# Kernel optimization log

Measured on AMD Instinct MI355X. Metric: run time of the kernel, lower is better.

Reference implementation:

```python
import jax, jax.numpy as jnp
import numpy as np

B, F, V, D, K = 16384, 39, 30000, 16, 20
EPS = 1e-5


def bn_eval(x, g, b):
    # inference-mode BatchNorm1d with running_mean=0, running_var=1
    return g * x / jnp.sqrt(1.0 + EPS) + b


def setup_inputs() -> dict:
    key = jax.random.key(0)
    ks = jax.random.split(key, 12)
    x = jax.random.randint(ks[0], (B, F), 0, V)
    emb_table = jax.random.normal(ks[1], (F * V, D), dtype=jnp.float32) * 0.05
    w_c = jax.random.normal(ks[2], (F, F * D), dtype=jnp.float32) * 0.05
    w0 = jax.random.normal(ks[3], (1024, F * D), dtype=jnp.float32) * 0.04
    w1 = jax.random.normal(ks[4], (512, 1024), dtype=jnp.float32) * 0.03
    w_out = jax.random.normal(ks[5], (1, 512), dtype=jnp.float32) * 0.04
    return {
        'x': x, 'emb_table': emb_table,
        'w_c': w_c, 'b_c': jnp.zeros((F,)), 'g_c': jnp.ones((F,)), 'be_c': jnp.zeros((F,)),
        'w0': w0, 'b0': jnp.zeros((1024,)), 'g0': jnp.ones((1024,)), 'be0': jnp.zeros((1024,)),
        'w1': w1, 'b1': jnp.zeros((512,)), 'g1': jnp.ones((512,)), 'be1': jnp.zeros((512,)),
        'w_out': w_out, 'b_out': jnp.zeros((1,)),
    }


def reference(x, emb_table, w_c, b_c, g_c, be_c, w0, b0, g0, be0,
              w1, b1, g1, be1, w_out, b_out):
    offsets = jnp.arange(F, dtype=x.dtype) * V          # per-field offsets
    idx = x + offsets[None, :]                          # [B, F]
    emb = emb_table[idx]                                # [B, F, D] gather

    # controller_mlp: flatten (batch, D, F) layout like torch transpose(1,2)
    flat = jnp.transpose(emb, (0, 2, 1)).reshape(B, F * D)
    h = jax.nn.relu(bn_eval(flat @ w_c.T + b_c, g_c, be_c))
    scores = jax.nn.softmax(h, axis=1)                  # [B, F]

    # kmax_pooling: top-k field indices, sorted ascending, gather weights
    _, kidx = jax.lax.top_k(scores, K)
    kidx = jnp.sort(kidx, axis=1)                       # [B, K]
    w = jnp.take_along_axis(scores, kidx, axis=1)       # [B, K]

    # forward_select: gather selected field embeddings, weight them
    sel = jnp.take_along_axis(emb, kidx[:, :, None], axis=1)  # [B, K, D]
    weighted = sel * w[:, :, None]

    # scatter back into full field slots (unselected fields are zero)
    full = jnp.zeros((B, F, D), weighted.dtype)
    bidx = jnp.arange(B)[:, None]
    full = full.at[bidx, kidx].set(weighted)            # [B, F, D]

    z = jnp.transpose(full, (0, 2, 1)).reshape(B, F * D)
    z = jax.nn.relu(bn_eval(z @ w0.T + b0, g0, be0))
    z = jax.nn.relu(bn_eval(z @ w1.T + b1, g1, be1))
    out = jax.nn.sigmoid(z @ w_out.T + b_out)           # [B, 1]
    return out.squeeze(-1)
```

## Files before the change

kernel.cpp:

```cpp
#include <hip/hip_runtime.h>
#include <math.h>

#define B_SZ 16384
#define F_N 39
#define V_N 30000
#define D_N 16
#define K_SEL 20
#define FD 624
#define KP0 640
#define NCP 48
#define N0 1024
#define N1 512
#define CBR 16
#define ALD 648

typedef unsigned short u16;
typedef __attribute__((ext_vector_type(8))) short bf16x8;
typedef __attribute__((ext_vector_type(8))) unsigned short u16x8;
typedef __attribute__((ext_vector_type(4))) float f32x4;
typedef __attribute__((ext_vector_type(4))) unsigned short u16x4;

__device__ __forceinline__ u16 f2bf(float v) {
    union { float f; unsigned u; } x; x.f = v;
    unsigned r = x.u + 0x7fff + ((x.u >> 16) & 1);
    return (u16)(r >> 16);
}
__device__ __forceinline__ float bf2f(u16 v) {
    union { unsigned u; float f; } x; x.u = ((unsigned)v) << 16;
    return x.f;
}
__device__ __forceinline__ unsigned cvtpk2(float a, float b) {
    unsigned d;
    asm("v_cvt_pk_bf16_f32 %0, %1, %2" : "=v"(d) : "v"(a), "v"(b));
    return d;
}

#define GLD16(gp, lp) __builtin_amdgcn_global_load_lds( \
    (const __attribute__((address_space(1))) unsigned int*)(gp), \
    (__attribute__((address_space(3))) unsigned int*)(lp), 16, 0, 0)

__global__ __launch_bounds__(256) void prep_all_kernel(
    const float* __restrict__ w0, const float* __restrict__ w1,
    const float* __restrict__ w_c, const float* __restrict__ b_c,
    const float* __restrict__ g_c, const float* __restrict__ be_c,
    u16* __restrict__ w0b, u16* __restrict__ w1b, u16* __restrict__ wcb,
    float* __restrict__ bcp, float* __restrict__ gcp, float* __restrict__ becp,
    float* __restrict__ outp)
{
    __shared__ float Lb[8][624];
    const int bid = blockIdx.x;
    const int t   = threadIdx.x;

    if (bid < 134) {
        const bool is_w0 = (bid < 128);
        const int r0 = is_w0 ? bid * 8 : (bid - 128) * 8;
        const int nrows_src = is_w0 ? N0 : F_N;
        const float* __restrict__ src = is_w0 ? w0 : w_c;
        u16* __restrict__ dst = is_w0 ? w0b : wcb;

        for (int j = t; j < 8 * 156; j += 256) {
            const int row = j / 156;
            const int c4  = j - row * 156;
            const int n   = r0 + row;
            if (n < nrows_src)
                *(float4*)&Lb[row][c4 * 4] =
                    *(const float4*)&src[(size_t)n * FD + c4 * 4];
        }
        __syncthreads();

        for (int j = t; j < 8 * 320; j += 256) {
            const int row = j / 320;
            const int pr  = j - row * 320;
            const int n   = r0 + row;
            const int k0  = pr * 2;
            float v0 = 0.f, v1 = 0.f;
            if (n < nrows_src) {
                const int d0 = k0 & 15,       f0 = k0 >> 4;
                const int d1 = (k0 + 1) & 15, f1 = (k0 + 1) >> 4;
                if (f0 < F_N) v0 = Lb[row][d0 * F_N + f0];
                if (f1 < F_N) v1 = Lb[row][d1 * F_N + f1];
            }
            *(unsigned*)&dst[(size_t)n * KP0 + k0] = cvtpk2(v0, v1);
        }
        return;
    }
    if (bid < 390) {
        const size_t e0 = (size_t)(bid - 134) * 2048 + t * 8;
        float4 v0 = *(const float4*)(w1 + e0);
        float4 v1 = *(const float4*)(w1 + e0 + 4);
        uint4 o = { cvtpk2(v0.x, v0.y), cvtpk2(v0.z, v0.w),
                    cvtpk2(v1.x, v1.y), cvtpk2(v1.z, v1.w) };
        *(uint4*)(w1b + e0) = o;
        return;
    }
    if (bid < 398) {
        const size_t e0 = (size_t)(bid - 390) * 2048 + t * 8;
        float4 z = {0.f, 0.f, 0.f, 0.f};
        *(float4*)(outp + e0)     = z;
        *(float4*)(outp + e0 + 4) = z;
        return;
    }
    if (t < 3 * NCP) {
        const int which = t / NCP, n = t - which * NCP;
        float v = 0.f;
        if (n < F_N) v = (which == 0) ? b_c[n] : (which == 1) ? g_c[n] : be_c[n];
        ((which == 0) ? bcp : (which == 1) ? gcp : becp)[n] = v;
    }
}

__global__ __launch_bounds__(256) void fused_controller_kernel(
    const int* __restrict__ x, const float* __restrict__ emb_table,
    const u16* __restrict__ wcb, const float* __restrict__ bcp,
    const float* __restrict__ gcp, const float* __restrict__ becp,
    u16* __restrict__ zb)
{
    __shared__ __align__(16) u16 Al[CBR * ALD];
    __shared__ float vv[CBR][49];
    __shared__ f32x4 part[4][64][3];
    __shared__ float selw[CBR][F_N];

    const int t    = threadIdx.x;
    const int wave = t >> 6;
    const int lane = t & 63;
    const int b0   = blockIdx.x * CBR;

    {
        const int p0 = t, p1 = t + 256, p2 = t + 512;
        const int xi0 = x[b0 * F_N + p0];
        const int xi1 = x[b0 * F_N + p1];
        const int xi2 = (p2 < CBR * F_N) ? x[b0 * F_N + p2] : 0;
        const int pp[3] = { p0, p1, p2 };
        const int xx[3] = { xi0, xi1, xi2 };
        #pragma unroll
        for (int s = 0; s < 3; ++s) {
            const int p = pp[s];
            if (p < CBR * F_N) {
                const int row = p / F_N;
                const int f   = p - row * F_N;
                const float4* src =
                    (const float4*)(emb_table + (size_t)(xx[s] + f * V_N) * D_N);
                float4 v0 = src[0], v1 = src[1], v2 = src[2], v3 = src[3];
                uint4 o0 = { cvtpk2(v0.x, v0.y), cvtpk2(v0.z, v0.w),
                             cvtpk2(v1.x, v1.y), cvtpk2(v1.z, v1.w) };
                uint4 o1 = { cvtpk2(v2.x, v2.y), cvtpk2(v2.z, v2.w),
                             cvtpk2(v3.x, v3.y), cvtpk2(v3.z, v3.w) };
                *(uint4*)&Al[row * ALD + f * D_N]     = o0;
                *(uint4*)&Al[row * ALD + f * D_N + 8] = o1;
            }
        }
    }
    __syncthreads();

    const int m = lane & 15;
    const int q = lane >> 4;
    f32x4 acc0 = {}, acc1 = {}, acc2 = {};
    {
        const u16* ap  = &Al[m * ALD + wave * 160 + q * 8];
        const u16* bp0 = wcb + (size_t)(0  + m) * KP0 + wave * 160 + q * 8;
        const u16* bp1 = wcb + (size_t)(16 + m) * KP0 + wave * 160 + q * 8;
        const u16* bp2 = wcb + (size_t)(32 + m) * KP0 + wave * 160 + q * 8;
        #pragma unroll
        for (int k = 0; k < 5; ++k) {
            bf16x8 af = *(const bf16x8*)ap;
            bf16x8 b0 = *(const bf16x8*)bp0;
            bf16x8 b1 = *(const bf16x8*)bp1;
            bf16x8 b2 = *(const bf16x8*)bp2;
            acc0 = __builtin_amdgcn_mfma_f32_16x16x32_bf16(af, b0, acc0, 0, 0, 0);
            acc1 = __builtin_amdgcn_mfma_f32_16x16x32_bf16(af, b1, acc1, 0, 0, 0);
            acc2 = __builtin_amdgcn_mfma_f32_16x16x32_bf16(af, b2, acc2, 0, 0, 0);
            ap += 32; bp0 += 32; bp1 += 32; bp2 += 32;
        }
    }
    part[wave][lane][0] = acc0;
    part[wave][lane][1] = acc1;
    part[wave][lane][2] = acc2;
    __syncthreads();

    {
        f32x4 r0 = part[0][lane][0] + part[1][lane][0] + part[2][lane][0] + part[3][lane][0];
        f32x4 r1 = part[0][lane][1] + part[1][lane][1] + part[2][lane][1] + part[3][lane][1];
        f32x4 r2 = part[0][lane][2] + part[1][lane][2] + part[2][lane][2] + part[3][lane][2];

        const float rs = rsqrtf(1.0f + 1e-5f);
        if (q == wave) {
            #pragma unroll
            for (int j = 0; j < 3; ++j) {
                const f32x4 a = (j == 0) ? r0 : (j == 1) ? r1 : r2;
                const int n = j * 16 + m;
                const float gn = gcp[n] * rs;
                const float bn = becp[n];
                const float bi = bcp[n];
                #pragma unroll
                for (int r = 0; r < 4; ++r)
                    vv[wave * 4 + r][n] = fmaxf(fmaf(gn, a[r] + bi, bn), 0.f);
            }
        }
    }
    __syncthreads();

    {
        const int row = wave * 4 + (lane >> 4);
        const int fl  = lane & 15;
        float e[3] = {0.f, 0.f, 0.f};
        float mloc = -1e30f;
        #pragma unroll
        for (int it = 0; it < 3; ++it) {
            const int f = fl + 16 * it;
            if (f < F_N) { e[it] = vv[row][f]; mloc = fmaxf(mloc, e[it]); }
        }
        mloc = fmaxf(mloc, __shfl_xor(mloc, 1, 64));
        mloc = fmaxf(mloc, __shfl_xor(mloc, 2, 64));
        mloc = fmaxf(mloc, __shfl_xor(mloc, 4, 64));
        mloc = fmaxf(mloc, __shfl_xor(mloc, 8, 64));
        float sloc = 0.f;
        #pragma unroll
        for (int it = 0; it < 3; ++it) {
            const int f = fl + 16 * it;
            if (f < F_N) { e[it] = expf(e[it] - mloc); sloc += e[it]; }
        }
        sloc += __shfl_xor(sloc, 1, 64);
        sloc += __shfl_xor(sloc, 2, 64);
        sloc += __shfl_xor(sloc, 4, 64);
        sloc += __shfl_xor(sloc, 8, 64);
        const float inv = 1.f / sloc;
        #pragma unroll
        for (int it = 0; it < 3; ++it) {
            const int f = fl + 16 * it;
            if (f < F_N) vv[row][f] = e[it];
        }

        int rank[3] = {};
        for (int gg = 0; gg < F_N; ++gg) {
            const float o = vv[row][gg];
            #pragma unroll
            for (int it = 0; it < 3; ++it) {
                const int f = fl + 16 * it;
                if (f < F_N)
                    rank[it] += (o > e[it] || (o == e[it] && gg < f)) ? 1 : 0;
            }
        }
        #pragma unroll
        for (int it = 0; it < 3; ++it) {
            const int f = fl + 16 * it;
            if (f < F_N)
                selw[row][f] = (rank[it] < K_SEL) ? e[it] * inv : 0.f;
        }
    }
    __syncthreads();

    for (int gp = t; gp < CBR * 40; gp += 256) {
        const int row  = gp / 40;
        const int slot = gp - row * 40;
        u16* dst = zb + (size_t)(b0 + row) * KP0 + slot * D_N;
        uint4 o0 = {0u,0u,0u,0u}, o1 = {0u,0u,0u,0u};
        if (slot < F_N) {
            const float w = selw[row][slot];
            u16x8 a0 = *(u16x8*)&Al[row * ALD + slot * D_N];
            u16x8 a1 = *(u16x8*)&Al[row * ALD + slot * D_N + 8];
            o0 = (uint4){ cvtpk2(bf2f(a0[0]) * w, bf2f(a0[1]) * w),
                          cvtpk2(bf2f(a0[2]) * w, bf2f(a0[3]) * w),
                          cvtpk2(bf2f(a0[4]) * w, bf2f(a0[5]) * w),
                          cvtpk2(bf2f(a0[6]) * w, bf2f(a0[7]) * w) };
            o1 = (uint4){ cvtpk2(bf2f(a1[0]) * w, bf2f(a1[1]) * w),
                          cvtpk2(bf2f(a1[2]) * w, bf2f(a1[3]) * w),
                          cvtpk2(bf2f(a1[4]) * w, bf2f(a1[5]) * w),
                          cvtpk2(bf2f(a1[6]) * w, bf2f(a1[7]) * w) };
        }
        *(uint4*)dst       = o0;
        *(uint4*)(dst + 8) = o1;
    }
}

template<int MODE>
__global__ __launch_bounds__(512) void gemm_mfma_bn_relu(
    const u16* __restrict__ A, const u16* __restrict__ W,
    const float* __restrict__ bias, const float* __restrict__ g,
    const float* __restrict__ be, u16* __restrict__ Cout,
    int M, int N, int Kp,
    const float* __restrict__ w_out, float* __restrict__ outp)
{
    __shared__ __align__(16) u16 SM[3 * 12288];

    const int t    = threadIdx.x;
    const int wave = t >> 6;
    const int lane = t & 63;
    const int wm   = wave >> 1, wn = wave & 1;
    const int m0   = blockIdx.x * 256;
    const int n0   = blockIdx.y * 128;

    const int rA0 = t >> 2;
    const int cA0 = (t & 3) ^ ((rA0 >> 1) & 3);
    const int rA1 = 128 + rA0;
    const int cA1 = (t & 3) ^ ((rA1 >> 1) & 3);
    const u16* gA0 = A + (size_t)(m0 + rA0) * Kp + cA0 * 8;
    const u16* gA1 = A + (size_t)(m0 + rA1) * Kp + cA1 * 8;
    const u16* gB  = W + (size_t)(n0 + rA0) * Kp + cA0 * 8;
    const int dA0 = t * 8, dA1 = 4096 + t * 8, dB = 8192 + t * 8;

    const int q    = lane >> 4;
    const int lr16 = lane & 15;

    int aoff[4], boff[4];
    #pragma unroll
    for (int i = 0; i < 4; ++i) {
        int ra = wm * 64 + i * 16 + lr16;
        aoff[i] = ra * 32 + ((q ^ ((ra >> 1) & 3)) * 8);
        int rb = wn * 64 + i * 16 + lr16;
        boff[i] = rb * 32 + ((q ^ ((rb >> 1) & 3)) * 8);
    }

    const int NIT = Kp >> 5;

    GLD16(gA0, SM + dA0);
    GLD16(gA1, SM + dA1);
    GLD16(gB,  SM + dB);
    gA0 += 32; gA1 += 32; gB += 32;
    GLD16(gA0, SM + 12288 + dA0);
    GLD16(gA1, SM + 12288 + dA1);
    GLD16(gB,  SM + 12288 + dB);
    gA0 += 32; gA1 += 32; gB += 32;

    f32x4 acc[4][4] = {};
    int cur = 0, stg = 2;

    for (int it = 0; it < NIT - 1; ++it) {
        asm volatile("s_waitcnt vmcnt(3)" ::: "memory");
        __builtin_amdgcn_s_barrier();
        __builtin_amdgcn_sched_barrier(0);

        const u16* ac = SM + cur * 12288;
        const u16* bc = ac + 8192;

        bf16x8 af0 = *(const bf16x8*)(ac + aoff[0]);
        bf16x8 af1 = *(const bf16x8*)(ac + aoff[1]);
        bf16x8 b0v = *(const bf16x8*)(bc + boff[0]);
        bf16x8 b1v = *(const bf16x8*)(bc + boff[1]);
        bf16x8 b2v = *(const bf16x8*)(bc + boff[2]);
        bf16x8 b3v = *(const bf16x8*)(bc + boff[3]);

        if (it + 2 < NIT) {
            u16* s = SM + stg * 12288;
            GLD16(gA0, s + dA0);
            GLD16(gA1, s + dA1);
            GLD16(gB,  s + dB);
            gA0 += 32; gA1 += 32; gB += 32;
        }

        asm volatile("s_waitcnt lgkmcnt(0)" ::: "memory");
        __builtin_amdgcn_sched_barrier(0);
        __builtin_amdgcn_s_setprio(1);
        acc[0][0] = __builtin_amdgcn_mfma_f32_16x16x32_bf16(af0, b0v, acc[0][0], 0, 0, 0);
        acc[0][1] = __builtin_amdgcn_mfma_f32_16x16x32_bf16(af0, b1v, acc[0][1], 0, 0, 0);
        acc[0][2] = __builtin_amdgcn_mfma_f32_16x16x32_bf16(af0, b2v, acc[0][2], 0, 0, 0);
        acc[0][3] = __builtin_amdgcn_mfma_f32_16x16x32_bf16(af0, b3v, acc[0][3], 0, 0, 0);
        acc[1][0] = __builtin_amdgcn_mfma_f32_16x16x32_bf16(af1, b0v, acc[1][0], 0, 0, 0);
        acc[1][1] = __builtin_amdgcn_mfma_f32_16x16x32_bf16(af1, b1v, acc[1][1], 0, 0, 0);
        acc[1][2] = __builtin_amdgcn_mfma_f32_16x16x32_bf16(af1, b2v, acc[1][2], 0, 0, 0);
        acc[1][3] = __builtin_amdgcn_mfma_f32_16x16x32_bf16(af1, b3v, acc[1][3], 0, 0, 0);
        __builtin_amdgcn_s_setprio(0);
        __builtin_amdgcn_s_barrier();

        bf16x8 af2 = *(const bf16x8*)(ac + aoff[2]);
        bf16x8 af3 = *(const bf16x8*)(ac + aoff[3]);
        asm volatile("s_waitcnt lgkmcnt(0)" ::: "memory");
        __builtin_amdgcn_sched_barrier(0);
        __builtin_amdgcn_s_setprio(1);
        acc[2][0] = __builtin_amdgcn_mfma_f32_16x16x32_bf16(af2, b0v, acc[2][0], 0, 0, 0);
        acc[2][1] = __builtin_amdgcn_mfma_f32_16x16x32_bf16(af2, b1v, acc[2][1], 0, 0, 0);
        acc[2][2] = __builtin_amdgcn_mfma_f32_16x16x32_bf16(af2, b2v, acc[2][2], 0, 0, 0);
        acc[2][3] = __builtin_amdgcn_mfma_f32_16x16x32_bf16(af2, b3v, acc[2][3], 0, 0, 0);
        acc[3][0] = __builtin_amdgcn_mfma_f32_16x16x32_bf16(af3, b0v, acc[3][0], 0, 0, 0);
        acc[3][1] = __builtin_amdgcn_mfma_f32_16x16x32_bf16(af3, b1v, acc[3][1], 0, 0, 0);
        acc[3][2] = __builtin_amdgcn_mfma_f32_16x16x32_bf16(af3, b2v, acc[3][2], 0, 0, 0);
        acc[3][3] = __builtin_amdgcn_mfma_f32_16x16x32_bf16(af3, b3v, acc[3][3], 0, 0, 0);
        __builtin_amdgcn_s_setprio(0);

        cur = (cur == 2) ? 0 : cur + 1;
        stg = (stg == 2) ? 0 : stg + 1;
    }

    asm volatile("s_waitcnt vmcnt(0)" ::: "memory");
    __builtin_amdgcn_s_barrier();
    __builtin_amdgcn_sched_barrier(0);
    {
        const u16* ac = SM + cur * 12288;
        const u16* bc = ac + 8192;
        bf16x8 af[4], bfr[4];
        #pragma unroll
        for (int i = 0; i < 4; ++i) af[i]  = *(const bf16x8*)(ac + aoff[i]);
        #pragma unroll
        for (int j = 0; j < 4; ++j) bfr[j] = *(const bf16x8*)(bc + boff[j]);
        __builtin_amdgcn_s_setprio(1);
        #pragma unroll
        for (int i = 0; i < 4; ++i)
            #pragma unroll
            for (int j = 0; j < 4; ++j)
                acc[i][j] = __builtin_amdgcn_mfma_f32_16x16x32_bf16(
                    af[i], bfr[j], acc[i][j], 0, 0, 0);
        __builtin_amdgcn_s_setprio(0);
    }

    const float rs = rsqrtf(1.0f + 1e-5f);
    if (MODE == 0) {
        __syncthreads();
        u16* Cs = SM;
        #pragma unroll
        for (int j = 0; j < 4; ++j) {
            const int nl = wn * 64 + j * 16 + lr16;
            const int n  = n0 + nl;
            const float bn_g = g[n] * rs;
            const float bn_b = be[n];
            const float bi   = bias[n];
            #pragma unroll
            for (int i = 0; i < 4; ++i) {
                const int mlb = wm * 64 + i * 16 + q * 4;
                float v0 = fmaxf(fmaf(bn_g, acc[i][j][0] + bi, bn_b), 0.f);
                float v1 = fmaxf(fmaf(bn_g, acc[i][j][1] + bi, bn_b), 0.f);
                float v2 = fmaxf(fmaf(bn_g, acc[i][j][2] + bi, bn_b), 0.f);
                float v3 = fmaxf(fmaf(bn_g, acc[i][j][3] + bi, bn_b), 0.f);
                unsigned pA = cvtpk2(v0, v1);
                unsigned pB = cvtpk2(v2, v3);
                Cs[(mlb + 0) * 136 + nl] = (u16)pA;
                Cs[(mlb + 1) * 136 + nl] = (u16)(pA >> 16);
                Cs[(mlb + 2) * 136 + nl] = (u16)pB;
                Cs[(mlb + 3) * 136 + nl] = (u16)(pB >> 16);
            }
        }
        __syncthreads();
        #pragma unroll
        for (int s = 0; s < 8; ++s) {
            const int chunk = s * 512 + t;
            const int row   = chunk >> 4;
            const int col   = (chunk & 15) << 3;
            *(u16x8*)&Cout[(size_t)(m0 + row) * N + n0 + col] =
                *(const u16x8*)&Cs[row * 136 + col];
        }
    } else {
        float s[4][4] = {};
        #pragma unroll
        for (int j = 0; j < 4; ++j) {
            const int n = n0 + wn * 64 + j * 16 + lr16;
            const float bn_g = g[n] * rs;
            const float bn_b = be[n];
            const float bi   = bias[n];
            const float wo   = w_out[n];
            #pragma unroll
            for (int i = 0; i < 4; ++i)
                #pragma unroll
                for (int r = 0; r < 4; ++r) {
                    float v = acc[i][j][r] + bi;
                    v = fmaxf(fmaf(bn_g, v, bn_b), 0.f);
                    s[i][r] = fmaf(v, wo, s[i][r]);
                }
        }
        #pragma unroll
        for (int i = 0; i < 4; ++i)
            #pragma unroll
            for (int r = 0; r < 4; ++r) {
                float v = s[i][r];
                v += __shfl_xor(v, 1, 64);
                v += __shfl_xor(v, 2, 64);
                v += __shfl_xor(v, 4, 64);
                v += __shfl_xor(v, 8, 64);
                s[i][r] = v;
            }
        if (lr16 == 0) {
            #pragma unroll
            for (int i = 0; i < 4; ++i) {
                const int mbase = m0 + wm * 64 + i * 16 + q * 4;
                #pragma unroll
                for (int r = 0; r < 4; ++r)
                    atomicAdd(&outp[mbase + r], s[i][r]);
            }
        }
    }
}

__global__ __launch_bounds__(256) void sigmoid_kernel(
    const float* __restrict__ outp, const float* __restrict__ b_out,
    float* __restrict__ out)
{
    const int b = blockIdx.x * 256 + threadIdx.x;
    out[b] = 1.f / (1.f + expf(-(outp[b] + b_out[0])));
}

extern "C" void kernel_launch(void* const* d_in, const int* in_sizes, int n_in,
                              void* d_out, int out_size, void* d_ws, size_t ws_size,
                              hipStream_t stream)
{
    const int*   x     = (const int*)  d_in[0];
    const float* emb   = (const float*)d_in[1];
    const float* w_c   = (const float*)d_in[2];
    const float* b_c   = (const float*)d_in[3];
    const float* g_c   = (const float*)d_in[4];
    const float* be_c  = (const float*)d_in[5];
    const float* w0    = (const float*)d_in[6];
    const float* b0    = (const float*)d_in[7];
    const float* g0    = (const float*)d_in[8];
    const float* be0   = (const float*)d_in[9];
    const float* w1    = (const float*)d_in[10];
    const float* b1    = (const float*)d_in[11];
    const float* g1    = (const float*)d_in[12];
    const float* be1   = (const float*)d_in[13];
    const float* w_out = (const float*)d_in[14];
    const float* b_out = (const float*)d_in[15];
    float* out = (float*)d_out;

    u16*   zb    = (u16*)d_ws;
    u16*   w0b   = zb    + (size_t)B_SZ * KP0;
    u16*   h0b   = w0b   + (size_t)N0 * KP0;
    u16*   w1b   = h0b   + (size_t)B_SZ * N0;
    u16*   wcb   = w1b   + (size_t)N1 * N0;
    float* outp  = (float*)(wcb + (size_t)NCP * KP0);
    float* bcp   = outp + B_SZ;
    float* gcp   = bcp + NCP;
    float* becp  = gcp + NCP;

    prep_all_kernel<<<399, 256, 0, stream>>>(
        w0, w1, w_c, b_c, g_c, be_c, w0b, w1b, wcb, bcp, gcp, becp, outp);

    fused_controller_kernel<<<B_SZ / CBR, 256, 0, stream>>>(
        x, emb, wcb, bcp, gcp, becp, zb);

    gemm_mfma_bn_relu<0><<<dim3(B_SZ / 256, N0 / 128), 512, 0, stream>>>(
        zb, w0b, b0, g0, be0, h0b, B_SZ, N0, KP0, nullptr, nullptr);

    gemm_mfma_bn_relu<1><<<dim3(B_SZ / 256, N1 / 128), 512, 0, stream>>>(
        h0b, w1b, b1, g1, be1, nullptr, B_SZ, N1, N0, w_out, outp);

    sigmoid_kernel<<<B_SZ / 256, 256, 0, stream>>>(outp, b_out, out);
}
```

Baseline: 205.6 us.

## Rewrite MLP GEMMs with larger tiles, K=64 stages and phased MFMA pipeline

Replaces the templated 256x128 GEMM with two specialised kernels. The first layer now uses 256x256 tiles and the second 256x128, both with 8 waves laid out 2x4, K-steps of 64, and double buffering. Global-to-LDS loads are split across several barrier-separated phases that are interleaved with MFMA bursts. The larger tiles raise reuse per byte loaded and the phasing overlaps loads with compute, at the cost of more accumulator registers, more LDS, and fewer blocks for the first layer (256).

Result: no change. 208.4 us (+1.4%).

```diff
diff --git a/kernel.cpp b/kernel.cpp
--- a/kernel.cpp
+++ b/kernel.cpp
@@ -18,13 +18,7 @@
 typedef __attribute__((ext_vector_type(8))) short bf16x8;
 typedef __attribute__((ext_vector_type(8))) unsigned short u16x8;
 typedef __attribute__((ext_vector_type(4))) float f32x4;
-typedef __attribute__((ext_vector_type(4))) unsigned short u16x4;
-
-__device__ __forceinline__ u16 f2bf(float v) {
-    union { float f; unsigned u; } x; x.f = v;
-    unsigned r = x.u + 0x7fff + ((x.u >> 16) & 1);
-    return (u16)(r >> 16);
-}
+
 __device__ __forceinline__ float bf2f(u16 v) {
     union { unsigned u; float f; } x; x.u = ((unsigned)v) << 16;
     return x.f;
@@ -38,6 +32,13 @@
 #define GLD16(gp, lp) __builtin_amdgcn_global_load_lds( \
     (const __attribute__((address_space(1))) unsigned int*)(gp), \
     (__attribute__((address_space(3))) unsigned int*)(lp), 16, 0, 0)
+
+#define MFMA16(a, b, c) __builtin_amdgcn_mfma_f32_16x16x32_bf16((a), (b), (c), 0, 0, 0)
+
+#define SBAR()   __builtin_amdgcn_s_barrier()
+#define SCHB()   __builtin_amdgcn_sched_barrier(0)
+#define LGKM0()  asm volatile("s_waitcnt lgkmcnt(0)" ::: "memory")
+#define PRIO(x)  __builtin_amdgcn_s_setprio(x)
 
 __global__ __launch_bounds__(256) void prep_all_kernel(
     const float* __restrict__ w0, const float* __restrict__ w1,
@@ -162,12 +163,12 @@
         #pragma unroll
         for (int k = 0; k < 5; ++k) {
             bf16x8 af = *(const bf16x8*)ap;
-            bf16x8 b0 = *(const bf16x8*)bp0;
-            bf16x8 b1 = *(const bf16x8*)bp1;
-            bf16x8 b2 = *(const bf16x8*)bp2;
-            acc0 = __builtin_amdgcn_mfma_f32_16x16x32_bf16(af, b0, acc0, 0, 0, 0);
-            acc1 = __builtin_amdgcn_mfma_f32_16x16x32_bf16(af, b1, acc1, 0, 0, 0);
-            acc2 = __builtin_amdgcn_mfma_f32_16x16x32_bf16(af, b2, acc2, 0, 0, 0);
+            bf16x8 b0r = *(const bf16x8*)bp0;
+            bf16x8 b1r = *(const bf16x8*)bp1;
+            bf16x8 b2r = *(const bf16x8*)bp2;
+            acc0 = MFMA16(af, b0r, acc0);
+            acc1 = MFMA16(af, b1r, acc1);
+            acc2 = MFMA16(af, b2r, acc2);
             ap += 32; bp0 += 32; bp1 += 32; bp2 += 32;
         }
     }
@@ -271,208 +272,341 @@
     }
 }
 
-template<int MODE>
-__global__ __launch_bounds__(512) void gemm_mfma_bn_relu(
+__global__ __launch_bounds__(512) void gemm0_8ph(
     const u16* __restrict__ A, const u16* __restrict__ W,
     const float* __restrict__ bias, const float* __restrict__ g,
-    const float* __restrict__ be, u16* __restrict__ Cout,
-    int M, int N, int Kp,
+    const float* __restrict__ be, u16* __restrict__ Cout)
+{
+    __shared__ __align__(16) u16 SM[2 * 32768];
+
+    const int t    = threadIdx.x;
+    const int lane = t & 63;
+    const int wave = t >> 6;
+    const int wm = wave >> 2, wn = wave & 3;
+    const int q = lane >> 4, lr16 = lane & 15;
+    const int m0 = blockIdx.x * 256;
+    const int n0 = blockIdx.y * 256;
+
+    const u16* gA[2]; const u16* gB[2];
+    int dA[2], dB[2];
+    #pragma unroll
+    for (int j = 0; j < 2; ++j) {
+        const int c  = t + j * 512;
+        const int lr = c >> 3;
+        const int ch = c & 7;
+        const int chg = ch ^ (lr & 7);
+        const int rA = lr + (lr & 64);
+        const int rB = (lr & 31) + ((lr >> 5) << 6);
+        gA[j] = A + (size_t)(m0 + rA) * KP0 + chg * 8;
+        gB[j] = W + (size_t)(n0 + rB) * KP0 + chg * 8;
+        dA[j] = rA * 64 + ch * 8;
+        dB[j] = 16384 + rB * 64 + ch * 8;
+    }
+
+    int aoff[4][2], boff[4][2];
+    #pragma unroll
+    for (int f = 0; f < 4; ++f)
+        #pragma unroll
+        for (int k = 0; k < 2; ++k) {
+            const int ra = wm * 128 + f * 16 + lr16;
+            aoff[f][k] = ra * 64 + (((k * 4 + q) ^ (lr16 & 7)) * 8);
+            const int rb = wn * 64 + f * 16 + lr16;
+            boff[f][k] = 16384 + rb * 64 + (((k * 4 + q) ^ (lr16 & 7)) * 8);
+        }
+
+    GLD16(gA[0],            SM + dA[0]);
+    GLD16(gA[1],            SM + dA[1]);
+    GLD16(gB[0],            SM + dB[0]);
+    GLD16(gB[1],            SM + dB[1]);
+    GLD16(gB[0] + 32 * KP0, SM + dB[0] + 2048);
+    GLD16(gB[1] + 32 * KP0, SM + dB[1] + 2048);
+    GLD16(gA[0] + 64 * KP0, SM + dA[0] + 4096);
+    GLD16(gA[1] + 64 * KP0, SM + dA[1] + 4096);
+
+    f32x4 acc[8][4] = {};
+    bf16x8 aR[4][2], bR[4][2];
+
+    for (int kt = 0; kt < 10; ++kt) {
+        const u16* sb = SM + (kt & 1) * 32768;
+        u16* nb = SM + ((kt & 1) ^ 1) * 32768;
+        const int ko = (kt + 1) * 64;
+        const bool more = (kt + 1 < 10);
+
+        asm volatile("s_waitcnt vmcnt(4)" ::: "memory");
+        SBAR(); SCHB();
+        #pragma unroll
+        for (int f = 0; f < 4; ++f)
+            #pragma unroll
+            for (int k = 0; k < 2; ++k)
+                aR[f][k] = *(const bf16x8*)(sb + aoff[f][k]);
+        #pragma unroll
+        for (int f = 0; f < 2; ++f)
+            #pragma unroll
+            for (int k = 0; k < 2; ++k)
+                bR[f][k] = *(const bf16x8*)(sb + boff[f][k]);
+        if (more) {
+            GLD16(gA[0] + ko, nb + dA[0]);
+            GLD16(gA[1] + ko, nb + dA[1]);
+        }
+        LGKM0(); SCHB(); PRIO(1);
+        #pragma unroll
+        for (int f = 0; f < 4; ++f)
+            #pragma unroll
+            for (int n = 0; n < 2; ++n) {
+                acc[f][n] = MFMA16(aR[f][0], bR[n][0], acc[f][n]);
+                acc[f][n] = MFMA16(aR[f][1], bR[n][1], acc[f][n]);
+            }
+        PRIO(0);
+
+        if (more) { asm volatile("s_waitcnt vmcnt(4)" ::: "memory"); }
+        else      { asm volatile("s_waitcnt vmcnt(2)" ::: "memory"); }
+        SBAR(); SCHB();
+        #pragma unroll
+        for (int f = 0; f < 2; ++f)
+            #pragma unroll
+            for (int k = 0; k < 2; ++k)
+                bR[2 + f][k] = *(const bf16x8*)(sb + boff[2 + f][k]);
+        if (more) {
+            GLD16(gB[0] + ko, nb + dB[0]);
+            GLD16(gB[1] + ko, nb + dB[1]);
+        }
+        LGKM0(); SCHB(); PRIO(1);
+        #pragma unroll
+        for (int f = 0; f < 4; ++f)
+            #pragma unroll
+            for (int n = 0; n < 2; ++n) {
+                acc[f][2 + n] = MFMA16(aR[f][0], bR[2 + n][0], acc[f][2 + n]);
+                acc[f][2 + n] = MFMA16(aR[f][1], bR[2 + n][1], acc[f][2 + n]);
+            }
+        PRIO(0);
+
+        if (more) { asm volatile("s_waitcnt vmcnt(4)" ::: "memory"); }
+        else      { asm volatile("s_waitcnt vmcnt(0)" ::: "memory"); }
+        SBAR(); SCHB();
+        #pragma unroll
+        for (int f = 0; f < 4; ++f)
+            #pragma unroll
+            for (int k = 0; k < 2; ++k)
+                aR[f][k] = *(const bf16x8*)(sb + aoff[f][k] + 4096);
+        if (more) {
+            GLD16(gB[0] + 32 * KP0 + ko, nb + dB[0] + 2048);
+            GLD16(gB[1] + 32 * KP0 + ko, nb + dB[1] + 2048);
+        }
+        LGKM0(); SCHB(); PRIO(1);
+        #pragma unroll
+        for (int f = 0; f < 4; ++f)
+            #pragma unroll
+            for (int n = 0; n < 2; ++n) {
+                acc[4 + f][2 + n] = MFMA16(aR[f][0], bR[2 + n][0], acc[4 + f][2 + n]);
+                acc[4 + f][2 + n] = MFMA16(aR[f][1], bR[2 + n][1], acc[4 + f][2 + n]);
+            }
+        PRIO(0);
+
+        if (more) {
+            GLD16(gA[0] + 64 * KP0 + ko, nb + dA[0] + 4096);
+            GLD16(gA[1] + 64 * KP0 + ko, nb + dA[1] + 4096);
+        }
+        PRIO(1);
+        #pragma unroll
+        for (int f = 0; f < 4; ++f)
+            #pragma unroll
+            for (int n = 0; n < 2; ++n) {
+                acc[4 + f][n] = MFMA16(aR[f][0], bR[n][0], acc[4 + f][n]);
+                acc[4 + f][n] = MFMA16(aR[f][1], bR[n][1], acc[4 + f][n]);
+            }
+        PRIO(0);
+    }
+
+    const float rs = rsqrtf(1.0f + 1e-5f);
+    __syncthreads();
+    u16* Cs = SM;
+    #pragma unroll
+    for (int rho = 0; rho < 2; ++rho) {
+        if (wm == rho) {
+            #pragma unroll
+            for (int nf = 0; nf < 4; ++nf) {
+                const int nl = wn * 64 + nf * 16 + lr16;
+                const int n  = n0 + nl;
+                const float bn_g = g[n] * rs;
+                const float bn_b = be[n];
+                const float bi   = bias[n];
+                #pragma unroll
+                for (int mf = 0; mf < 8; ++mf) {
+                    const int rb = mf * 16 + q * 4;
+                    float v0 = fmaxf(fmaf(bn_g, acc[mf][nf][0] + bi, bn_b), 0.f);
+                    float v1 = fmaxf(fmaf(bn_g, acc[mf][nf][1] + bi, bn_b), 0.f);
+                    float v2 = fmaxf(fmaf(bn_g, acc[mf][nf][2] + bi, bn_b), 0.f);
+                    float v3 = fmaxf(fmaf(bn_g, acc[mf][nf][3] + bi, bn_b), 0.f);
+                    unsigned pa = cvtpk2(v0, v1);
+                    unsigned pb = cvtpk2(v2, v3);
+                    Cs[(rb + 0) * 264 + nl] = (u16)pa;
+                    Cs[(rb + 1) * 264 + nl] = (u16)(pa >> 16);
+                    Cs[(rb + 2) * 264 + nl] = (u16)pb;
+                    Cs[(rb + 3) * 264 + nl] = (u16)(pb >> 16);
+                }
+            }
+        }
+        __syncthreads();
+        #pragma unroll
+        for (int s = 0; s < 8; ++s) {
+            const int chunk = s * 512 + t;
+            const int row   = chunk >> 5;
+            const int col   = (chunk & 31) << 3;
+            *(u16x8*)&Cout[(size_t)(m0 + rho * 128 + row) * N0 + n0 + col] =
+                *(const u16x8*)&Cs[row * 264 + col];
+        }
+        __syncthreads();
+    }
+}
+
+__global__ __launch_bounds__(512) void gemm1_8ph(
+    const u16* __restrict__ A, const u16* __restrict__ W,
+    const float* __restrict__ bias, const float* __restrict__ g,
+    const float* __restrict__ be,
     const float* __restrict__ w_out, float* __restrict__ outp)
 {
-    __shared__ __align__(16) u16 SM[3 * 12288];
+    __shared__ __align__(16) u16 SM[2 * 24576];
 
     const int t    = threadIdx.x;
+    const int lane = t & 63;
     const int wave = t >> 6;
-    const int lane = t & 63;
-    const int wm   = wave >> 1, wn = wave & 1;
-    const int m0   = blockIdx.x * 256;
-    const int n0   = blockIdx.y * 128;
-
-    const int rA0 = t >> 2;
-    const int cA0 = (t & 3) ^ ((rA0 >> 1) & 3);
-    const int rA1 = 128 + rA0;
-    const int cA1 = (t & 3) ^ ((rA1 >> 1) & 3);
-    const u16* gA0 = A + (size_t)(m0 + rA0) * Kp + cA0 * 8;
-    const u16* gA1 = A + (size_t)(m0 + rA1) * Kp + cA1 * 8;
-    const u16* gB  = W + (size_t)(n0 + rA0) * Kp + cA0 * 8;
-    const int dA0 = t * 8, dA1 = 4096 + t * 8, dB = 8192 + t * 8;
-
-    const int q    = lane >> 4;
-    const int lr16 = lane & 15;
-
-    int aoff[4], boff[4];
-    #pragma unroll
-    for (int i = 0; i < 4; ++i) {
-        int ra = wm * 64 + i * 16 + lr16;
-        aoff[i] = ra * 32 + ((q ^ ((ra >> 1) & 3)) * 8);
-        int rb = wn * 64 + i * 16 + lr16;
-        boff[i] = rb * 32 + ((q ^ ((rb >> 1) & 3)) * 8);
-    }
-
-    const int NIT = Kp >> 5;
-
-    GLD16(gA0, SM + dA0);
-    GLD16(gA1, SM + dA1);
-    GLD16(gB,  SM + dB);
-    gA0 += 32; gA1 += 32; gB += 32;
-    GLD16(gA0, SM + 12288 + dA0);
-    GLD16(gA1, SM + 12288 + dA1);
-    GLD16(gB,  SM + 12288 + dB);
-    gA0 += 32; gA1 += 32; gB += 32;
-
-    f32x4 acc[4][4] = {};
-    int cur = 0, stg = 2;
-
-    for (int it = 0; it < NIT - 1; ++it) {
-        asm volatile("s_waitcnt vmcnt(3)" ::: "memory");
-        __builtin_amdgcn_s_barrier();
-        __builtin_amdgcn_sched_barrier(0);
-
-        const u16* ac = SM + cur * 12288;
-        const u16* bc = ac + 8192;
-
-        bf16x8 af0 = *(const bf16x8*)(ac + aoff[0]);
-        bf16x8 af1 = *(const bf16x8*)(ac + aoff[1]);
-        bf16x8 b0v = *(const bf16x8*)(bc + boff[0]);
-        bf16x8 b1v = *(const bf16x8*)(bc + boff[1]);
-        bf16x8 b2v = *(const bf16x8*)(bc + boff[2]);
-        bf16x8 b3v = *(const bf16x8*)(bc + boff[3]);
-
-        if (it + 2 < NIT) {
-            u16* s = SM + stg * 12288;
-            GLD16(gA0, s + dA0);
-            GLD16(gA1, s + dA1);
-            GLD16(gB,  s + dB);
-            gA0 += 32; gA1 += 32; gB += 32;
-        }
-
-        asm volatile("s_waitcnt lgkmcnt(0)" ::: "memory");
-        __builtin_amdgcn_sched_barrier(0);
-        __builtin_amdgcn_s_setprio(1);
-        acc[0][0] = __builtin_amdgcn_mfma_f32_16x16x32_bf16(af0, b0v, acc[0][0], 0, 0, 0);
-        acc[0][1] = __builtin_amdgcn_mfma_f32_16x16x32_bf16(af0, b1v, acc[0][1], 0, 0, 0);
-        acc[0][2] = __builtin_amdgcn_mfma_f32_16x16x32_bf16(af0, b2v, acc[0][2], 0, 0, 0);
-        acc[0][3] = __builtin_amdgcn_mfma_f32_16x16x32_bf16(af0, b3v, acc[0][3], 0, 0, 0);
-        acc[1][0] = __builtin_amdgcn_mfma_f32_16x16x32_bf16(af1, b0v, acc[1][0], 0, 0, 0);
-        acc[1][1] = __builtin_amdgcn_mfma_f32_16x16x32_bf16(af1, b1v, acc[1][1], 0, 0, 0);
-        acc[1][2] = __builtin_amdgcn_mfma_f32_16x16x32_bf16(af1, b2v, acc[1][2], 0, 0, 0);
-        acc[1][3] = __builtin_amdgcn_mfma_f32_16x16x32_bf16(af1, b3v, acc[1][3], 0, 0, 0);
-        __builtin_amdgcn_s_setprio(0);
-        __builtin_amdgcn_s_barrier();
-
-        bf16x8 af2 = *(const bf16x8*)(ac + aoff[2]);
-        bf16x8 af3 = *(const bf16x8*)(ac + aoff[3]);
-        asm volatile("s_waitcnt lgkmcnt(0)" ::: "memory");
-        __builtin_amdgcn_sched_barrier(0);
-        __builtin_amdgcn_s_setprio(1);
-        acc[2][0] = __builtin_amdgcn_mfma_f32_16x16x32_bf16(af2, b0v, acc[2][0], 0, 0, 0);
-        acc[2][1] = __builtin_amdgcn_mfma_f32_16x16x32_bf16(af2, b1v, acc[2][1], 0, 0, 0);
-        acc[2][2] = __builtin_amdgcn_mfma_f32_16x16x32_bf16(af2, b2v, acc[2][2], 0, 0, 0);
-        acc[2][3] = __builtin_amdgcn_mfma_f32_16x16x32_bf16(af2, b3v, acc[2][3], 0, 0, 0);
-        acc[3][0] = __builtin_amdgcn_mfma_f32_16x16x32_bf16(af3, b0v, acc[3][0], 0, 0, 0);
-        acc[3][1] = __builtin_amdgcn_mfma_f32_16x16x32_bf16(af3, b1v, acc[3][1], 0, 0, 0);
-        acc[3][2] = __builtin_amdgcn_mfma_f32_16x16x32_bf16(af3, b2v, acc[3][2], 0, 0, 0);
-        acc[3][3] = __builtin_amdgcn_mfma_f32_16x16x32_bf16(af3, b3v, acc[3][3], 0, 0, 0);
-        __builtin_amdgcn_s_setprio(0);
-
-        cur = (cur == 2) ? 0 : cur + 1;
-        stg = (stg == 2) ? 0 : stg + 1;
-    }
-
-    asm volatile("s_waitcnt vmcnt(0)" ::: "memory");
-    __builtin_amdgcn_s_barrier();
-    __builtin_amdgcn_sched_barrier(0);
-    {
-        const u16* ac = SM + cur * 12288;
-        const u16* bc = ac + 8192;
-        bf16x8 af[4], bfr[4];
-        #pragma unroll
-        for (int i = 0; i < 4; ++i) af[i]  = *(const bf16x8*)(ac + aoff[i]);
-        #pragma unroll
-        for (int j = 0; j < 4; ++j) bfr[j] = *(const bf16x8*)(bc + boff[j]);
-        __builtin_amdgcn_s_setprio(1);
-        #pragma unroll
-        for (int i = 0; i < 4; ++i)
-            #pragma unroll
-            for (int j = 0; j < 4; ++j)
-                acc[i][j] = __builtin_amdgcn_mfma_f32_16x16x32_bf16(
-                    af[i], bfr[j], acc[i][j], 0, 0, 0);
-        __builtin_amdgcn_s_setprio(0);
+    const int wm = wave >> 2, wn = wave & 3;
+    const int q = lane >> 4, lr16 = lane & 15;
+    const int m0 = blockIdx.x * 256;
+    const int n0 = blockIdx.y * 128;
+
+    const u16* gA[2]; const u16* gB[2];
+    int dA[2], dB[2];
+    #pragma unroll
+    for (int j = 0; j < 2; ++j) {
+        const int c  = t + j * 512;
+        const int lr = c >> 3;
+        const int ch = c & 7;
+        const int chg = ch ^ (lr & 7);
+        const int rA = lr + (lr & 64);
+        gA[j] = A + (size_t)(m0 + rA) * N0 + chg * 8;
+        gB[j] = W + (size_t)(n0 + lr) * N0 + chg * 8;
+        dA[j] = rA * 64 + ch * 8;
+        dB[j] = 16384 + lr * 64 + ch * 8;
+    }
+
+    int aoff[4][2], boff[2][2];
+    #pragma unroll
+    for (int f = 0; f < 4; ++f)
+        #pragma unroll
+        for (int k = 0; k < 2; ++k) {
+            const int ra = wm * 128 + f * 16 + lr16;
+            aoff[f][k] = ra * 64 + (((k * 4 + q) ^ (lr16 & 7)) * 8);
+        }
+    #pragma unroll
+    for (int f = 0; f < 2; ++f)
+        #pragma unroll
+        for (int k = 0; k < 2; ++k) {
+            const int rb = wn * 32 + f * 16 + lr16;
+            boff[f][k] = 16384 + rb * 64 + (((k * 4 + q) ^ (lr16 & 7)) * 8);
+        }
+
+    GLD16(gA[0],           SM + dA[0]);
+    GLD16(gA[1],           SM + dA[1]);
+    GLD16(gB[0],           SM + dB[0]);
+    GLD16(gB[1],           SM + dB[1]);
+    GLD16(gA[0] + 64 * N0, SM + dA[0] + 4096);
+    GLD16(gA[1] + 64 * N0, SM + dA[1] + 4096);
+
+    f32x4 acc[8][2] = {};
+    bf16x8 aR[4][2], bR[2][2];
+
+    for (int kt = 0; kt < 16; ++kt) {
+        const u16* sb = SM + (kt & 1) * 24576;
+        u16* nb = SM + ((kt & 1) ^ 1) * 24576;
+        const int ko = (kt + 1) * 64;
+        const bool more = (kt + 1 < 16);
+
+        asm volatile("s_waitcnt vmcnt(2)" ::: "memory");
+        SBAR(); SCHB();
+        #pragma unroll
+        for (int f = 0; f < 4; ++f)
+            #pragma unroll
+            for (int k = 0; k < 2; ++k)
+                aR[f][k] = *(const bf16x8*)(sb + aoff[f][k]);
+        #pragma unroll
+        for (int f = 0; f < 2; ++f)
+            #pragma unroll
+            for (int k = 0; k < 2; ++k)
+                bR[f][k] = *(const bf16x8*)(sb + boff[f][k]);
+        if (more) {
+            GLD16(gA[0] + ko, nb + dA[0]);
+            GLD16(gA[1] + ko, nb + dA[1]);
+            GLD16(gB[0] + ko, nb + dB[0]);
+            GLD16(gB[1] + ko, nb + dB[1]);
+        }
+        LGKM0(); SCHB(); PRIO(1);
+        #pragma unroll
+        for (int f = 0; f < 4; ++f)
+            #pragma unroll
+            for (int n = 0; n < 2; ++n) {
+                acc[f][n] = MFMA16(aR[f][0], bR[n][0], acc[f][n]);
+                acc[f][n] = MFMA16(aR[f][1], bR[n][1], acc[f][n]);
+            }
+        PRIO(0);
+
+        if (more) { asm volatile("s_waitcnt vmcnt(4)" ::: "memory"); }
+        else      { asm volatile("s_waitcnt vmcnt(0)" ::: "memory"); }
+        SBAR(); SCHB();
+        #pragma unroll
+        for (int f = 0; f < 4; ++f)
+            #pragma unroll
+            for (int k = 0; k < 2; ++k)
+                aR[f][k] = *(const bf16x8*)(sb + aoff[f][k] + 4096);
+        if (more) {
+            GLD16(gA[0] + 64 * N0 + ko, nb + dA[0] + 4096);
+            GLD16(gA[1] + 64 * N0 + ko, nb + dA[1] + 4096);
+        }
+        LGKM0(); SCHB(); PRIO(1);
+        #pragma unroll
+        for (int f = 0; f < 4; ++f)
+            #pragma unroll
+            for (int n = 0; n < 2; ++n) {
+                acc[4 + f][n] = MFMA16(aR[f][0], bR[n][0], acc[4 + f][n]);
+                acc[4 + f][n] = MFMA16(aR[f][1], bR[n][1], acc[4 + f][n]);
+            }
+        PRIO(0);
     }
 
     const float rs = rsqrtf(1.0f + 1e-5f);
-    if (MODE == 0) {
-        __syncthreads();
-        u16* Cs = SM;
-        #pragma unroll
-        for (int j = 0; j < 4; ++j) {
-            const int nl = wn * 64 + j * 16 + lr16;
-            const int n  = n0 + nl;
-            const float bn_g = g[n] * rs;
-            const float bn_b = be[n];
-            const float bi   = bias[n];
-            #pragma unroll
-            for (int i = 0; i < 4; ++i) {
-                const int mlb = wm * 64 + i * 16 + q * 4;
-                float v0 = fmaxf(fmaf(bn_g, acc[i][j][0] + bi, bn_b), 0.f);
-                float v1 = fmaxf(fmaf(bn_g, acc[i][j][1] + bi, bn_b), 0.f);
-                float v2 = fmaxf(fmaf(bn_g, acc[i][j][2] + bi, bn_b), 0.f);
-                float v3 = fmaxf(fmaf(bn_g, acc[i][j][3] + bi, bn_b), 0.f);
-                unsigned pA = cvtpk2(v0, v1);
-                unsigned pB = cvtpk2(v2, v3);
-                Cs[(mlb + 0) * 136 + nl] = (u16)pA;
-                Cs[(mlb + 1) * 136 + nl] = (u16)(pA >> 16);
-                Cs[(mlb + 2) * 136 + nl] = (u16)pB;
-                Cs[(mlb + 3) * 136 + nl] = (u16)(pB >> 16);
-            }
-        }
-        __syncthreads();
-        #pragma unroll
-        for (int s = 0; s < 8; ++s) {
-            const int chunk = s * 512 + t;
-            const int row   = chunk >> 4;
-            const int col   = (chunk & 15) << 3;
-            *(u16x8*)&Cout[(size_t)(m0 + row) * N + n0 + col] =
-                *(const u16x8*)&Cs[row * 136 + col];
-        }
-    } else {
-        float s[4][4] = {};
-        #pragma unroll
-        for (int j = 0; j < 4; ++j) {
-            const int n = n0 + wn * 64 + j * 16 + lr16;
-            const float bn_g = g[n] * rs;
-            const float bn_b = be[n];
-            const float bi   = bias[n];
-            const float wo   = w_out[n];
-            #pragma unroll
-            for (int i = 0; i < 4; ++i)
-                #pragma unroll
-                for (int r = 0; r < 4; ++r) {
-                    float v = acc[i][j][r] + bi;
-                    v = fmaxf(fmaf(bn_g, v, bn_b), 0.f);
-                    s[i][r] = fmaf(v, wo, s[i][r]);
-                }
-        }
-        #pragma unroll
-        for (int i = 0; i < 4; ++i)
+    float s[8][4] = {};
+    #pragma unroll
+    for (int nf = 0; nf < 2; ++nf) {
+        const int n = n0 + wn * 32 + nf * 16 + lr16;
+        const float bn_g = g[n] * rs;
+        const float bn_b = be[n];
+        const float bi   = bias[n];
+        const float wo   = w_out[n];
+        #pragma unroll
+        for (int mf = 0; mf < 8; ++mf)
             #pragma unroll
             for (int r = 0; r < 4; ++r) {
-                float v = s[i][r];
-                v += __shfl_xor(v, 1, 64);
-                v += __shfl_xor(v, 2, 64);
-                v += __shfl_xor(v, 4, 64);
-                v += __shfl_xor(v, 8, 64);
-                s[i][r] = v;
-            }
-        if (lr16 == 0) {
-            #pragma unroll
-            for (int i = 0; i < 4; ++i) {
-                const int mbase = m0 + wm * 64 + i * 16 + q * 4;
-                #pragma unroll
-                for (int r = 0; r < 4; ++r)
-                    atomicAdd(&outp[mbase + r], s[i][r]);
-            }
-        }
+                float v = fmaxf(fmaf(bn_g, acc[mf][nf][r] + bi, bn_b), 0.f);
+                s[mf][r] = fmaf(v, wo, s[mf][r]);
+            }
+    }
+    #pragma unroll
+    for (int mf = 0; mf < 8; ++mf)
+        #pragma unroll
+        for (int r = 0; r < 4; ++r) {
+            float v = s[mf][r];
+            v += __shfl_xor(v, 1, 64);
+            v += __shfl_xor(v, 2, 64);
+            v += __shfl_xor(v, 4, 64);
+            v += __shfl_xor(v, 8, 64);
+            s[mf][r] = v;
+        }
+    if (lr16 == 0) {
+        #pragma unroll
+        for (int mf = 0; mf < 8; ++mf)
+            #pragma unroll
+            for (int r = 0; r < 4; ++r)
+                atomicAdd(&outp[m0 + wm * 128 + mf * 16 + q * 4 + r], s[mf][r]);
     }
 }
 
@@ -522,11 +656,11 @@
     fused_controller_kernel<<<B_SZ / CBR, 256, 0, stream>>>(
         x, emb, wcb, bcp, gcp, becp, zb);
 
-    gemm_mfma_bn_relu<0><<<dim3(B_SZ / 256, N0 / 128), 512, 0, stream>>>(
-        zb, w0b, b0, g0, be0, h0b, B_SZ, N0, KP0, nullptr, nullptr);
-
-    gemm_mfma_bn_relu<1><<<dim3(B_SZ / 256, N1 / 128), 512, 0, stream>>>(
-        h0b, w1b, b1, g1, be1, nullptr, B_SZ, N1, N0, w_out, outp);
+    gemm0_8ph<<<dim3(B_SZ / 256, N0 / 256), 512, 0, stream>>>(
+        zb, w0b, b0, g0, be0, h0b);
+
+    gemm1_8ph<<<dim3(B_SZ / 256, N1 / 128), 512, 0, stream>>>(
+        h0b, w1b, b1, g1, be1, w_out, outp);
 
     sigmoid_kernel<<<B_SZ / 256, 256, 0, stream>>>(outp, b_out, out);
 }
```
